# Kernel optimization log

Measured on AMD Instinct MI355X. Metric: run time of the kernel, lower is better.

Reference implementation:

```python
import jax, jax.numpy as jnp
import numpy as np

B, T, V, E, U = 256, 512, 20000, 128, 128


def setup_inputs() -> dict:
    key = jax.random.key(0)
    k = jax.random.split(key, 7)
    tokens = jax.random.randint(k[0], (B, T), 0, V)
    emb_table = jax.random.normal(k[1], (V, E), jnp.float32) * 0.05
    kernel = jax.random.normal(k[2], (E, 4 * U), jnp.float32) * 0.05
    recurrent_kernel = jax.random.normal(k[3], (U, 4 * U), jnp.float32) * 0.05
    # Keras default: unit_forget_bias -> forget-gate bias = 1, others 0 (gate order i,f,c,o)
    bias = jnp.concatenate([jnp.zeros(U), jnp.ones(U), jnp.zeros(2 * U)]).astype(jnp.float32)
    dense_w = jax.random.normal(k[4], (U, 1), jnp.float32) * 0.05
    dense_b = jnp.zeros((1,), jnp.float32)
    return {"tokens": tokens, "emb_table": emb_table, "kernel": kernel,
            "recurrent_kernel": recurrent_kernel, "bias": bias,
            "dense_w": dense_w, "dense_b": dense_b}


def reference(tokens, emb_table, kernel, recurrent_kernel, bias, dense_w, dense_b):
    # Embedding lookup: [B,T] -> [B,T,E]
    x = emb_table[tokens]
    # Precompute input projections for all timesteps: [B,T,4U]
    zx = jnp.einsum('bte,eg->btg', x, kernel) + bias

    def step(carry, z_t):
        h, c = carry
        z = z_t + h @ recurrent_kernel          # [B,4U]
        i, f, g, o = jnp.split(z, 4, axis=-1)   # Keras gate order i,f,c,o
        i = jax.nn.sigmoid(i)
        f = jax.nn.sigmoid(f)
        g = jnp.tanh(g)
        o = jax.nn.sigmoid(o)
        c = f * c + i * g
        h = o * jnp.tanh(c)
        return (h, c), None

    h0 = jnp.zeros((tokens.shape[0], U), zx.dtype)
    c0 = jnp.zeros((tokens.shape[0], U), zx.dtype)
    (h_final, _), _ = jax.lax.scan(step, (h0, c0), jnp.swapaxes(zx, 0, 1))
    # Dense sigmoid head: [B,1]
    return jax.nn.sigmoid(h_final @ dense_w + dense_b)
```

## Files before the change

### kernel.cpp

```cpp
#include <hip/hip_runtime.h>
#include <hip/hip_bf16.h>

#define BB 256
#define TT 512
#define VV 20000
#define EE 128
#define UU 128
#define G4 512

typedef _Float16 f16x8 __attribute__((ext_vector_type(8)));
typedef float    f32x4 __attribute__((ext_vector_type(4)));

__device__ __forceinline__ float sigmoid_f(float x) {
    float e = __expf(-x);
    return __builtin_amdgcn_rcpf(1.0f + e);
}
__device__ __forceinline__ float tanh_f(float x) {
    float e = __expf(2.0f * x);
    return 1.0f - 2.0f * __builtin_amdgcn_rcpf(e + 1.0f);
}

__global__ __launch_bounds__(512, 2) void proj_kernel(
    const float* __restrict__ emb, const float* __restrict__ wk,
    const float* __restrict__ bias, float* __restrict__ P) {
    const int col = threadIdx.x;
    const int v0  = blockIdx.x * 16;

    __shared__ float elds[16 * EE];
    ((float4*)elds)[col] = ((const float4*)(emb + (size_t)v0 * EE))[col];
    __syncthreads();

    float bcol = bias[col];
    float acc[16];
#pragma unroll
    for (int r = 0; r < 16; ++r) acc[r] = bcol;

    const float4* elds4 = (const float4*)elds;
    for (int e0 = 0; e0 < EE; e0 += 4) {
        float k0 = wk[(e0 + 0) * G4 + col];
        float k1 = wk[(e0 + 1) * G4 + col];
        float k2 = wk[(e0 + 2) * G4 + col];
        float k3 = wk[(e0 + 3) * G4 + col];
#pragma unroll
        for (int r = 0; r < 16; ++r) {
            float4 ev = elds4[r * 32 + (e0 >> 2)];
            acc[r] = fmaf(ev.x, k0, acc[r]);
            acc[r] = fmaf(ev.y, k1, acc[r]);
            acc[r] = fmaf(ev.z, k2, acc[r]);
            acc[r] = fmaf(ev.w, k3, acc[r]);
        }
    }
#pragma unroll
    for (int r = 0; r < 16; ++r)
        P[(size_t)(v0 + r) * G4 + col] = acc[r];
}

__global__ __launch_bounds__(512, 2) void lstm_kernel(
    const int* __restrict__ tokens, const float* __restrict__ rk,
    const float* __restrict__ P, const float* __restrict__ dense_w,
    const float* __restrict__ dense_b, float* __restrict__ out) {
    const int tid = threadIdx.x;
    const int w   = tid >> 6;
    const int l   = tid & 63;
    const int j   = l & 15;
    const int kq  = l >> 4;
    const int b   = blockIdx.x;
    const int ucol = 16 * w + j;

    __shared__ __align__(16) _Float16 hbuf[2][UU];
    __shared__ int   tokLDS[TT];
    __shared__ float red[8];

    f16x8 bf[4][4];
#pragma unroll
    for (int kt = 0; kt < 4; ++kt) {
#pragma unroll
        for (int g = 0; g < 4; ++g) {
            f16x8 v;
#pragma unroll
            for (int i = 0; i < 8; ++i) {
                v[i] = (_Float16)rk[(size_t)(32 * kt + 8 * kq + i) * G4
                                    + g * 128 + ucol];
            }
            bf[kt][g] = v;
        }
    }

    const int* trow = tokens + (size_t)b * TT;
    tokLDS[tid] = trow[tid];
    if (tid < UU) hbuf[0][tid] = (_Float16)0.f;
    float c_state = 0.f, hv = 0.f;

    const float* Pcol = P + (size_t)kq * 128 + ucol;
    float pf[4];
#pragma unroll
    for (int s = 0; s < 4; ++s) pf[s] = Pcol[(size_t)trow[s] * G4];
    __syncthreads();

    const f32x4 cz = {0.f, 0.f, 0.f, 0.f};

    for (int t = 0; t < TT; t += 4) {
#pragma unroll
        for (int s = 0; s < 4; ++s) {
            int tki  = t + s + 4; if (tki > TT - 1) tki = TT - 1;
            int vtok = tokLDS[tki];

            f16x8 af[4];
#pragma unroll
            for (int kt = 0; kt < 4; ++kt)
                af[kt] = *(const f16x8*)&hbuf[s & 1][32 * kt + 8 * kq];

            f32x4 acc[4];
#pragma unroll
            for (int g = 0; g < 4; ++g)
                acc[g] = __builtin_amdgcn_mfma_f32_16x16x32_f16(af[0], bf[0][g], cz, 0, 0, 0);
#pragma unroll
            for (int kt = 1; kt < 4; ++kt) {
#pragma unroll
                for (int g = 0; g < 4; ++g)
                    acc[g] = __builtin_amdgcn_mfma_f32_16x16x32_f16(af[kt], bf[kt][g], acc[g], 0, 0, 0);
            }

            float z0 = acc[0][0], z1 = acc[1][0], z2 = acc[2][0], z3 = acc[3][0];
            float zl = (kq & 2) ? ((kq & 1) ? z3 : z2) : ((kq & 1) ? z1 : z0);
            zl += pf[s];

            float xs = (kq == 2) ? zl + zl : zl;
            float sg = sigmoid_f(xs);
            float a  = (kq == 2) ? fmaf(2.f, sg, -1.f) : sg;

            float fa = __shfl(a, j + 16, 64);
            float ga = __shfl(a, j + 32, 64);
            float oa = __shfl(a, j + 48, 64);

            c_state = fmaf(fa, c_state, a * ga);
            hv      = oa * tanh_f(c_state);

            if (kq == 0) hbuf[(s + 1) & 1][ucol] = (_Float16)hv;

            pf[s] = Pcol[(size_t)vtok * G4];

            asm volatile("s_waitcnt lgkmcnt(0)" ::: "memory");
            __builtin_amdgcn_s_barrier();
        }
    }

    float val = (kq == 0) ? hv * dense_w[ucol] : 0.f;
#pragma unroll
    for (int off = 32; off > 0; off >>= 1) val += __shfl_xor(val, off, 64);
    if (l == 0) red[w] = val;
    __syncthreads();
    if (tid == 0) {
        float sum = dense_b[0];
#pragma unroll
        for (int i = 0; i < 8; ++i) sum += red[i];
        out[b] = sigmoid_f(sum);
    }
}

extern "C" void kernel_launch(void* const* d_in, const int* in_sizes, int n_in,
                              void* d_out, int out_size, void* d_ws, size_t ws_size,
                              hipStream_t stream) {
    const int*   tokens = (const int*)  d_in[0];
    const float* emb    = (const float*)d_in[1];
    const float* wk     = (const float*)d_in[2];
    const float* rk     = (const float*)d_in[3];
    const float* bias   = (const float*)d_in[4];
    const float* dw     = (const float*)d_in[5];
    const float* db     = (const float*)d_in[6];
    float* out = (float*)d_out;
    float* P   = (float*)d_ws;

    proj_kernel<<<VV / 16, 512, 0, stream>>>(emb, wk, bias, P);
    lstm_kernel<<<BB, 512, 0, stream>>>(tokens, rk, P, dw, db, out);
}
```

Measured before the change: 289.5 us.

## Interleave gate projections per unit and split MFMA chains to drop shuffles

```diff
diff --git a/kernel.cpp b/kernel.cpp
--- a/kernel.cpp
+++ b/kernel.cpp
@@ -22,12 +22,15 @@
 
 __global__ __launch_bounds__(512, 2) void proj_kernel(
     const float* __restrict__ emb, const float* __restrict__ wk,
-    const float* __restrict__ bias, float* __restrict__ P) {
-    const int col = threadIdx.x;
+    const float* __restrict__ bias, float* __restrict__ P2) {
+    const int tid = threadIdx.x;
+    const int g   = tid & 3;
+    const int u   = tid >> 2;
+    const int col = g * 128 + u;
     const int v0  = blockIdx.x * 16;
 
     __shared__ float elds[16 * EE];
-    ((float4*)elds)[col] = ((const float4*)(emb + (size_t)v0 * EE))[col];
+    ((float4*)elds)[tid] = ((const float4*)(emb + (size_t)v0 * EE))[tid];
     __syncthreads();
 
     float bcol = bias[col];
@@ -52,12 +55,12 @@
     }
 #pragma unroll
     for (int r = 0; r < 16; ++r)
-        P[(size_t)(v0 + r) * G4 + col] = acc[r];
+        P2[(size_t)(v0 + r) * G4 + tid] = acc[r];
 }
 
 __global__ __launch_bounds__(512, 2) void lstm_kernel(
     const int* __restrict__ tokens, const float* __restrict__ rk,
-    const float* __restrict__ P, const float* __restrict__ dense_w,
+    const float* __restrict__ P2, const float* __restrict__ dense_w,
     const float* __restrict__ dense_b, float* __restrict__ out) {
     const int tid = threadIdx.x;
     const int w   = tid >> 6;
@@ -91,10 +94,10 @@
     if (tid < UU) hbuf[0][tid] = (_Float16)0.f;
     float c_state = 0.f, hv = 0.f;
 
-    const float* Pcol = P + (size_t)kq * 128 + ucol;
-    float pf[4];
+    const float4* Pc4 = (const float4*)(P2 + (size_t)ucol * 4);
+    float4 pf[4];
 #pragma unroll
-    for (int s = 0; s < 4; ++s) pf[s] = Pcol[(size_t)trow[s] * G4];
+    for (int s = 0; s < 4; ++s) pf[s] = Pc4[(size_t)trow[s] * 128];
     __syncthreads();
 
     const f32x4 cz = {0.f, 0.f, 0.f, 0.f};
@@ -110,35 +113,34 @@
             for (int kt = 0; kt < 4; ++kt)
                 af[kt] = *(const f16x8*)&hbuf[s & 1][32 * kt + 8 * kq];
 
-            f32x4 acc[4];
+            float4 pnew = Pc4[(size_t)vtok * 128];
+
+            f32x4 accA[4], accB[4];
 #pragma unroll
-            for (int g = 0; g < 4; ++g)
-                acc[g] = __builtin_amdgcn_mfma_f32_16x16x32_f16(af[0], bf[0][g], cz, 0, 0, 0);
+            for (int g = 0; g < 4; ++g) {
+                accA[g] = __builtin_amdgcn_mfma_f32_16x16x32_f16(af[0], bf[0][g], cz, 0, 0, 0);
+                accB[g] = __builtin_amdgcn_mfma_f32_16x16x32_f16(af[2], bf[2][g], cz, 0, 0, 0);
+            }
 #pragma unroll
-            for (int kt = 1; kt < 4; ++kt) {
-#pragma unroll
-                for (int g = 0; g < 4; ++g)
-                    acc[g] = __builtin_amdgcn_mfma_f32_16x16x32_f16(af[kt], bf[kt][g], acc[g], 0, 0, 0);
+            for (int g = 0; g < 4; ++g) {
+                accA[g] = __builtin_amdgcn_mfma_f32_16x16x32_f16(af[1], bf[1][g], accA[g], 0, 0, 0);
+                accB[g] = __builtin_amdgcn_mfma_f32_16x16x32_f16(af[3], bf[3][g], accB[g], 0, 0, 0);
             }
 
-            float z0 = acc[0][0], z1 = acc[1][0], z2 = acc[2][0], z3 = acc[3][0];
-            float zl = (kq & 2) ? ((kq & 1) ? z3 : z2) : ((kq & 1) ? z1 : z0);
-            zl += pf[s];
+            float z0 = accA[0][0] + accB[0][0] + pf[s].x;
+            float z1 = accA[1][0] + accB[1][0] + pf[s].y;
+            float z2 = accA[2][0] + accB[2][0] + pf[s].z;
+            float z3 = accA[3][0] + accB[3][0] + pf[s].w;
 
-            float xs = (kq == 2) ? zl + zl : zl;
-            float sg = sigmoid_f(xs);
-            float a  = (kq == 2) ? fmaf(2.f, sg, -1.f) : sg;
-
-            float fa = __shfl(a, j + 16, 64);
-            float ga = __shfl(a, j + 32, 64);
-            float oa = __shfl(a, j + 48, 64);
-
-            c_state = fmaf(fa, c_state, a * ga);
-            hv      = oa * tanh_f(c_state);
+            float gi = sigmoid_f(z0);
+            float gf = sigmoid_f(z1);
+            float gg = tanh_f(z2);
+            float go = sigmoid_f(z3);
+            c_state = fmaf(gf, c_state, gi * gg);
+            hv      = go * tanh_f(c_state);
 
             if (kq == 0) hbuf[(s + 1) & 1][ucol] = (_Float16)hv;
-
-            pf[s] = Pcol[(size_t)vtok * G4];
+            pf[s] = pnew;
 
             asm volatile("s_waitcnt lgkmcnt(0)" ::: "memory");
             __builtin_amdgcn_s_barrier();
@@ -169,8 +171,8 @@
     const float* dw     = (const float*)d_in[5];
     const float* db     = (const float*)d_in[6];
     float* out = (float*)d_out;
-    float* P   = (float*)d_ws;
+    float* P2  = (float*)d_ws;
 
-    proj_kernel<<<VV / 16, 512, 0, stream>>>(emb, wk, bias, P);
-    lstm_kernel<<<BB, 512, 0, stream>>>(tokens, rk, P, dw, db, out);
+    proj_kernel<<<VV / 16, 512, 0, stream>>>(emb, wk, bias, P2);
+    lstm_kernel<<<BB, 512, 0, stream>>>(tokens, rk, P2, dw, db, out);
 }
```

Result: no change. 289.8 us (+0.1%).
